# Performance work log

Hardware: AMD Instinct MI355X
Metric: run time of the kernel (lower is better)

## Reference

```python
import jax, jax.numpy as jnp
import numpy as np

N, E, D = 10000, 160000, 512
H, C = 4, 128          # hidden layers: 4 heads x 128 = 512 (residual-compatible)
HF, CF = 2, 512        # final layer: 2 heads, concat=False (mean)
NEG_SLOPE = 0.2


def _gat(x, src, dst, W, a_src, a_dst, b, heads, out_c, concat):
    """PyG-style GATConv (v1 attention), no dropout (eval mode)."""
    n = x.shape[0]
    h = (x @ W).reshape(n, heads, out_c)                  # [N,H,C]
    es = (h * a_src).sum(-1)                              # [N,H]
    ed = (h * a_dst).sum(-1)                              # [N,H]
    e = jax.nn.leaky_relu(es[src] + ed[dst], NEG_SLOPE)   # [E,H]
    m = jax.ops.segment_max(e, dst, num_segments=n)       # softmax over in-edges of dst
    m = jnp.where(jnp.isfinite(m), m, 0.0)                # guard isolated nodes
    ex = jnp.exp(e - m[dst])
    den = jax.ops.segment_sum(ex, dst, num_segments=n)
    alpha = ex / (den[dst] + 1e-16)                       # [E,H]
    msg = h[src] * alpha[..., None]                       # [E,H,C]
    out = jax.ops.segment_sum(msg, dst, num_segments=n)   # [N,H,C]
    out = out.reshape(n, heads * out_c) if concat else out.mean(axis=1)
    return out + b


def setup_inputs() -> dict:
    key = jax.random.key(0)
    ks = jax.random.split(key, 16)
    s = 0.05
    return {
        "graph": jax.random.normal(ks[0], (N, D), jnp.float32),
        "edge_index": jax.random.randint(ks[1], (2, E), 0, N, dtype=jnp.int32),
        "W1": jax.random.normal(ks[2], (D, H * C), jnp.float32) * s,
        "as1": jax.random.normal(ks[3], (H, C), jnp.float32) * s,
        "ad1": jax.random.normal(ks[4], (H, C), jnp.float32) * s,
        "b1": jnp.zeros((H * C,), jnp.float32),
        "W2": jax.random.normal(ks[5], (H * C, H * C), jnp.float32) * s,
        "as2": jax.random.normal(ks[6], (H, C), jnp.float32) * s,
        "ad2": jax.random.normal(ks[7], (H, C), jnp.float32) * s,
        "b2": jnp.zeros((H * C,), jnp.float32),
        "W3": jax.random.normal(ks[8], (H * C, HF * CF), jnp.float32) * s,
        "as3": jax.random.normal(ks[9], (HF, CF), jnp.float32) * s,
        "ad3": jax.random.normal(ks[10], (HF, CF), jnp.float32) * s,
        "b3": jnp.zeros((CF,), jnp.float32),
    }


def reference(graph, edge_index, W1, as1, ad1, b1, W2, as2, ad2, b2, W3, as3, ad3, b3):
    src, dst = edge_index[0], edge_index[1]
    # layer_size=2: conv1 + convs[0] with ELU+residual, convs[1] (concat=False) residual only
    x = jax.nn.elu(_gat(graph, src, dst, W1, as1, ad1, b1, H, C, True) + graph)
    x = jax.nn.elu(_gat(x, src, dst, W2, as2, ad2, b2, H, C, True) + x)
    x = _gat(x, src, dst, W3, as3, ad3, b3, HF, CF, False) + x
    return x
```

## Files before the change

kernel.cpp:

```cpp
#include <hip/hip_runtime.h>
#include <hip/hip_bf16.h>
#include <hip/hip_fp16.h>
#include <cstddef>
#include <cstdint>


typedef _Float16 half8 __attribute__((ext_vector_type(8)));
typedef _Float16 half4v __attribute__((ext_vector_type(4)));
typedef float floatx4 __attribute__((ext_vector_type(4)));

#define AS1(p) ((const __attribute__((address_space(1))) void*)(p))
#define AS3(p) ((__attribute__((address_space(3))) void*)(p))

__device__ __forceinline__ float leaky_exp(float e) {
    e = (e > 0.f) ? e : 0.2f * e;
    return __expf(e);
}


__global__ void count_deg(const int* __restrict__ dst, int* __restrict__ deg, int E) {
    int e = blockIdx.x * blockDim.x + threadIdx.x;
    if (e < E) atomicAdd(&deg[dst[e]], 1);
}

__global__ void scan_kernel(const int* __restrict__ deg, int* __restrict__ row_start,
                            int* __restrict__ cursor, int n) {
    __shared__ int wsum[16];
    __shared__ int carry_s;
    int tid = threadIdx.x;
    int wave = tid >> 6, lane = tid & 63;
    if (tid == 0) { carry_s = 0; row_start[0] = 0; }
    __syncthreads();
    for (int base = 0; base < n; base += 1024) {
        int i = base + tid;
        int v = (i < n) ? deg[i] : 0;
        int x = v;
#pragma unroll
        for (int off = 1; off < 64; off <<= 1) {
            int t = __shfl_up(x, off);
            if (lane >= off) x += t;
        }
        if (lane == 63) wsum[wave] = x;
        __syncthreads();
        if (wave == 0 && lane < 16) {
            int w = wsum[lane];
#pragma unroll
            for (int off = 1; off < 16; off <<= 1) {
                int t = __shfl_up(w, off);
                if (lane >= off) w += t;
            }
            wsum[lane] = w;
        }
        __syncthreads();
        int carry = carry_s;
        int incl = x + (wave ? wsum[wave - 1] : 0) + carry;
        if (i < n) { row_start[i + 1] = incl; cursor[i] = incl - v; }
        __syncthreads();
        if (tid == 1023) carry_s = incl;
        __syncthreads();
    }
}

__global__ void scatter_edges(const int* __restrict__ src, const int* __restrict__ dst,
                              int* __restrict__ cursor, int* __restrict__ srcs, int E) {
    int e = blockIdx.x * blockDim.x + threadIdx.x;
    if (e < E) {
        int p = atomicAdd(&cursor[dst[e]], 1);
        srcs[p] = src[e];
    }
}


__global__ void cast_f16(const float* __restrict__ in, _Float16* __restrict__ out, int n4) {
    int i = blockIdx.x * blockDim.x + threadIdx.x;
    if (i < n4) {
        float4 v = ((const float4*)in)[i];
        half4v o = {(_Float16)v.x, (_Float16)v.y, (_Float16)v.z, (_Float16)v.w};
        ((half4v*)out)[i] = o;
    }
}

__global__ void prep_weights(const float* __restrict__ W1, const float* __restrict__ W2,
                             const float* __restrict__ W3,
                             _Float16* __restrict__ Wt1, _Float16* __restrict__ Wt2,
                             _Float16* __restrict__ Bt3) {
    __shared__ float t[32][33];
    int b = blockIdx.x;
    int region = b >> 8, idx = b & 255;
    int r0 = (idx >> 4) * 32, c0 = (idx & 15) * 32;
    const float* in;
    _Float16* out;
    int in_ld, out_ld;
    if (region == 0)      { in = W1;       out = Wt1;       in_ld = 512;  out_ld = 512;  }
    else if (region == 1) { in = W2;       out = Wt2;       in_ld = 512;  out_ld = 512;  }
    else if (region == 2) { in = W3;       out = Bt3;       in_ld = 1024; out_ld = 1024; }
    else                  { in = W3 + 512; out = Bt3 + 512; in_ld = 1024; out_ld = 1024; }
    int tx = threadIdx.x, ty = threadIdx.y;
    for (int i = ty; i < 32; i += 8)
        t[i][tx] = in[(size_t)(r0 + i) * in_ld + c0 + tx];
    __syncthreads();
    for (int i = ty; i < 32; i += 8)
        out[(size_t)(c0 + i) * out_ld + r0 + tx] = (_Float16)t[tx][i];
}

__global__ void proj_all(const float* __restrict__ W1, const float* __restrict__ as1,
                         const float* __restrict__ ad1,
                         const float* __restrict__ W2, const float* __restrict__ as2,
                         const float* __restrict__ ad2,
                         const float* __restrict__ W3, const float* __restrict__ as3,
                         const float* __restrict__ ad3,
                         _Float16* __restrict__ Wt1, _Float16* __restrict__ Wt2,
                         float* __restrict__ wes3, float* __restrict__ wed3) {
    int w = (blockIdx.x * blockDim.x + threadIdx.x) >> 6;
    int lane = threadIdx.x & 63;
    if (w < 8192) {
        int layer = w >> 12;
        int idx = w & 4095;
        int d = idx & 511, hh = (idx >> 9) & 3, sel = idx >> 11;
        const float* W = layer ? W2 : W1;
        const float* a = layer ? (sel ? ad2 : as2) : (sel ? ad1 : as1);
        const float* row = W + (size_t)d * 512 + hh * 128;
        const float* av = a + hh * 128;
        float s = 0.f;
        s += row[lane] * av[lane];
        s += row[lane + 64] * av[lane + 64];
#pragma unroll
        for (int off = 32; off; off >>= 1) s += __shfl_down(s, off);
        if (lane == 0) {
            _Float16* Wt = layer ? Wt2 : Wt1;
            Wt[(size_t)(512 + sel * 4 + hh) * 512 + d] = (_Float16)s;
        }
    } else if (w < 10240) {
        int idx = w - 8192;
        int k = idx & 511, hh = (idx >> 9) & 1, sel = idx >> 10;
        const float* a = (sel ? ad3 : as3) + hh * 512;
        const float* row = W3 + (size_t)k * 1024 + hh * 512;
        float s = 0.f;
        for (int c = lane; c < 512; c += 64) s += row[c] * a[c];
#pragma unroll
        for (int off = 32; off; off >>= 1) s += __shfl_down(s, off);
        if (lane == 0) (sel ? wed3 : wes3)[hh * 512 + k] = s;
    } else if (w < 11136) {
        int z = (w - 10240) * 64 + lane;
        int layer = z / 28672;
        int rem = z - layer * 28672;
        int row = 520 + rem / 512, col = rem & 511;
        (layer ? Wt2 : Wt1)[(size_t)row * 512 + col] = (_Float16)0.f;
    }
}


#define BK 64

__global__ __launch_bounds__(256) void gemm_f16_att(const _Float16* __restrict__ A,
                                                    const _Float16* __restrict__ Bt,
                                                    _Float16* __restrict__ Hout,
                                                    float* __restrict__ es,
                                                    float* __restrict__ ed,
                                                    int M, int K) {
    __shared__ _Float16 As[64 * BK];
    __shared__ _Float16 Bs[64 * BK];
    int tid = threadIdx.x;
    int lane = tid & 63, wave = tid >> 6;
    int wm = (wave & 1) * 32, wn = (wave >> 1) * 32;
    int m0 = blockIdx.y * 64, n0 = blockIdx.x * 64;
    int l15 = lane & 15, quad = lane >> 4;
    int trow = tid >> 3, tcol = tid & 7;

    floatx4 acc[2][2];
#pragma unroll
    for (int i = 0; i < 2; ++i)
#pragma unroll
        for (int j = 0; j < 2; ++j) acc[i][j] = (floatx4){0.f, 0.f, 0.f, 0.f};

    for (int k0 = 0; k0 < K; k0 += BK) {
        __syncthreads();
#pragma unroll
        for (int i = 0; i < 2; ++i) {
            int gr = m0 + i * 32 + trow; if (gr >= M) gr = M - 1;
            __builtin_amdgcn_global_load_lds(AS1(A + (size_t)gr * K + k0 + tcol * 8),
                                             AS3(As + (size_t)(i * 256 + tid) * 8), 16, 0, 0);
        }
#pragma unroll
        for (int i = 0; i < 2; ++i) {
            int gr = n0 + i * 32 + trow;
            __builtin_amdgcn_global_load_lds(AS1(Bt + (size_t)gr * K + k0 + tcol * 8),
                                             AS3(Bs + (size_t)(i * 256 + tid) * 8), 16, 0, 0);
        }
        __syncthreads();
#pragma unroll
        for (int ks = 0; ks < BK; ks += 32) {
            half8 af[2], bfr[2];
#pragma unroll
            for (int i = 0; i < 2; ++i)
                af[i] = *(const half8*)&As[(wm + i * 16 + l15) * BK + ks + quad * 8];
#pragma unroll
            for (int j = 0; j < 2; ++j)
                bfr[j] = *(const half8*)&Bs[(wn + j * 16 + l15) * BK + ks + quad * 8];
#pragma unroll
            for (int i = 0; i < 2; ++i)
#pragma unroll
                for (int j = 0; j < 2; ++j)
                    acc[i][j] = __builtin_amdgcn_mfma_f32_16x16x32_f16(af[i], bfr[j], acc[i][j], 0, 0, 0);
        }
    }
#pragma unroll
    for (int i = 0; i < 2; ++i)
#pragma unroll
        for (int j = 0; j < 2; ++j) {
            int col = n0 + wn + j * 16 + l15;
#pragma unroll
            for (int r = 0; r < 4; ++r) {
                int row = m0 + wm + i * 16 + quad * 4 + r;
                if (row < M) {
                    float v = acc[i][j][r];
                    if (col < 512) Hout[(size_t)row * 512 + col] = (_Float16)v;
                    else if (col < 516) es[row * 4 + col - 512] = v;
                    else if (col < 520) ed[row * 4 + col - 516] = v;
                }
            }
        }
}

__global__ __launch_bounds__(256) void gemm_f16_ep(const _Float16* __restrict__ A,
                                                   const _Float16* __restrict__ Bt,
                                                   float* __restrict__ out,
                                                   const float* __restrict__ bias,
                                                   const _Float16* __restrict__ xres,
                                                   int M, int Nn, int K) {
    __shared__ _Float16 As[64 * BK];
    __shared__ _Float16 Bs[64 * BK];
    int tid = threadIdx.x;
    int lane = tid & 63, wave = tid >> 6;
    int wm = (wave & 1) * 32, wn = (wave >> 1) * 32;
    int m0 = blockIdx.y * 64, n0 = blockIdx.x * 64;
    int l15 = lane & 15, quad = lane >> 4;
    int trow = tid >> 3, tcol = tid & 7;

    floatx4 acc[2][2];
#pragma unroll
    for (int i = 0; i < 2; ++i)
#pragma unroll
        for (int j = 0; j < 2; ++j) acc[i][j] = (floatx4){0.f, 0.f, 0.f, 0.f};

    for (int k0 = 0; k0 < K; k0 += BK) {
        __syncthreads();
#pragma unroll
        for (int i = 0; i < 2; ++i) {
            int gr = m0 + i * 32 + trow; if (gr >= M) gr = M - 1;
            __builtin_amdgcn_global_load_lds(AS1(A + (size_t)gr * K + k0 + tcol * 8),
                                             AS3(As + (size_t)(i * 256 + tid) * 8), 16, 0, 0);
        }
#pragma unroll
        for (int i = 0; i < 2; ++i) {
            int gr = n0 + i * 32 + trow;
            __builtin_amdgcn_global_load_lds(AS1(Bt + (size_t)gr * K + k0 + tcol * 8),
                                             AS3(Bs + (size_t)(i * 256 + tid) * 8), 16, 0, 0);
        }
        __syncthreads();
#pragma unroll
        for (int ks = 0; ks < BK; ks += 32) {
            half8 af[2], bfr[2];
#pragma unroll
            for (int i = 0; i < 2; ++i)
                af[i] = *(const half8*)&As[(wm + i * 16 + l15) * BK + ks + quad * 8];
#pragma unroll
            for (int j = 0; j < 2; ++j)
                bfr[j] = *(const half8*)&Bs[(wn + j * 16 + l15) * BK + ks + quad * 8];
#pragma unroll
            for (int i = 0; i < 2; ++i)
#pragma unroll
                for (int j = 0; j < 2; ++j)
                    acc[i][j] = __builtin_amdgcn_mfma_f32_16x16x32_f16(af[i], bfr[j], acc[i][j], 0, 0, 0);
        }
    }
#pragma unroll
    for (int i = 0; i < 2; ++i)
#pragma unroll
        for (int j = 0; j < 2; ++j) {
            int col = n0 + wn + j * 16 + l15;
#pragma unroll
            for (int r = 0; r < 4; ++r) {
                int row = m0 + wm + i * 16 + quad * 4 + r;
                if (row < M)
                    out[(size_t)row * Nn + col] =
                        0.5f * acc[i][j][r] + bias[col] + (float)xres[(size_t)row * Nn + col];
            }
        }
}


template <bool RES32, bool COEF3>
__global__ __launch_bounds__(512) void aggregate7_concat(
    const _Float16* __restrict__ h, const float* __restrict__ es,
    const float* __restrict__ ed,
    const int* __restrict__ row_start, const int* __restrict__ srcs,
    const float* __restrict__ bias, const float* __restrict__ xres32,
    const _Float16* __restrict__ xres16, _Float16* __restrict__ x_out_h,
    const float* __restrict__ wes3, const float* __restrict__ wed3,
    float* __restrict__ es3, float* __restrict__ ed3, int Nn) {
    int wave = threadIdx.x >> 6, lane = threadIdx.x & 63;
    int n = blockIdx.x * 8 + wave;
    if (n >= Nn) return;
    int head = lane >> 4;
    int c0 = lane * 8;
    float edn = ed[n * 4 + head];
    int beg = row_start[n], end = row_start[n + 1];
    float acc[8] = {};
    float den = 0.f;
    int j = beg;
    for (; j + 3 < end; j += 4) {
        int s0 = srcs[j], s1 = srcs[j + 1], s2 = srcs[j + 2], s3 = srcs[j + 3];
        float e0 = es[s0 * 4 + head], e1 = es[s1 * 4 + head];
        float e2 = es[s2 * 4 + head], e3 = es[s3 * 4 + head];
        half8 h0 = *(const half8*)&h[(size_t)s0 * 512 + c0];
        half8 h1 = *(const half8*)&h[(size_t)s1 * 512 + c0];
        half8 h2 = *(const half8*)&h[(size_t)s2 * 512 + c0];
        half8 h3 = *(const half8*)&h[(size_t)s3 * 512 + c0];
        float w0 = leaky_exp(e0 + edn), w1 = leaky_exp(e1 + edn);
        float w2 = leaky_exp(e2 + edn), w3 = leaky_exp(e3 + edn);
        den += w0 + w1 + w2 + w3;
#pragma unroll
        for (int k = 0; k < 8; ++k) acc[k] += w0 * (float)h0[k];
#pragma unroll
        for (int k = 0; k < 8; ++k) acc[k] += w1 * (float)h1[k];
#pragma unroll
        for (int k = 0; k < 8; ++k) acc[k] += w2 * (float)h2[k];
#pragma unroll
        for (int k = 0; k < 8; ++k) acc[k] += w3 * (float)h3[k];
    }
    for (; j < end; ++j) {
        int s = srcs[j];
        float w = leaky_exp(es[s * 4 + head] + edn);
        half8 hv = *(const half8*)&h[(size_t)s * 512 + c0];
        den += w;
#pragma unroll
        for (int k = 0; k < 8; ++k) acc[k] += w * (float)hv[k];
    }
    float invden = 1.f / (den + 1e-16f);
    size_t base = (size_t)n * 512 + c0;
    float v[8];
    half8 o;
#pragma unroll
    for (int k = 0; k < 8; ++k) {
        float res = RES32 ? xres32[base + k] : (float)xres16[base + k];
        float t = acc[k] * invden + bias[c0 + k] + res;
        t = (t > 0.f) ? t : expm1f(t);
        v[k] = t;
        o[k] = (_Float16)t;
    }
    *(half8*)&x_out_h[base] = o;
    if (COEF3) {
        float t0 = 0.f, t1 = 0.f, t2 = 0.f, t3 = 0.f;
#pragma unroll
        for (int k = 0; k < 8; ++k) {
            t0 += v[k] * wes3[c0 + k];
            t1 += v[k] * wes3[512 + c0 + k];
            t2 += v[k] * wed3[c0 + k];
            t3 += v[k] * wed3[512 + c0 + k];
        }
#pragma unroll
        for (int off = 32; off; off >>= 1) {
            t0 += __shfl_down(t0, off);
            t1 += __shfl_down(t1, off);
            t2 += __shfl_down(t2, off);
            t3 += __shfl_down(t3, off);
        }
        if (lane == 0) {
            es3[n * 2] = t0; es3[n * 2 + 1] = t1;
            ed3[n * 2] = t2; ed3[n * 2 + 1] = t3;
        }
    }
}


__global__ __launch_bounds__(512) void aggregate7_dual(
    const _Float16* __restrict__ x, const float* __restrict__ es3,
    const float* __restrict__ ed3,
    const int* __restrict__ row_start, const int* __restrict__ srcs,
    _Float16* __restrict__ y, int Nn) {
    int wave = threadIdx.x >> 6, lane = threadIdx.x & 63;
    int n = blockIdx.x * 8 + wave;
    if (n >= Nn) return;
    int c0 = lane * 8;
    float edn0 = ed3[n * 2], edn1 = ed3[n * 2 + 1];
    int beg = row_start[n], end = row_start[n + 1];
    float a0[8] = {}, a1[8] = {};
    float den0 = 0.f, den1 = 0.f;
    int j = beg;
    for (; j + 3 < end; j += 4) {
        int s0 = srcs[j], s1 = srcs[j + 1], s2 = srcs[j + 2], s3 = srcs[j + 3];
        float2 q0 = *(const float2*)&es3[s0 * 2];
        float2 q1 = *(const float2*)&es3[s1 * 2];
        float2 q2 = *(const float2*)&es3[s2 * 2];
        float2 q3 = *(const float2*)&es3[s3 * 2];
        half8 h0 = *(const half8*)&x[(size_t)s0 * 512 + c0];
        half8 h1 = *(const half8*)&x[(size_t)s1 * 512 + c0];
        half8 h2 = *(const half8*)&x[(size_t)s2 * 512 + c0];
        half8 h3 = *(const half8*)&x[(size_t)s3 * 512 + c0];
        float u0 = leaky_exp(q0.x + edn0), v0 = leaky_exp(q0.y + edn1);
        float u1 = leaky_exp(q1.x + edn0), v1 = leaky_exp(q1.y + edn1);
        float u2 = leaky_exp(q2.x + edn0), v2 = leaky_exp(q2.y + edn1);
        float u3 = leaky_exp(q3.x + edn0), v3 = leaky_exp(q3.y + edn1);
        den0 += u0 + u1 + u2 + u3;
        den1 += v0 + v1 + v2 + v3;
#pragma unroll
        for (int k = 0; k < 8; ++k) { float f = (float)h0[k]; a0[k] += u0 * f; a1[k] += v0 * f; }
#pragma unroll
        for (int k = 0; k < 8; ++k) { float f = (float)h1[k]; a0[k] += u1 * f; a1[k] += v1 * f; }
#pragma unroll
        for (int k = 0; k < 8; ++k) { float f = (float)h2[k]; a0[k] += u2 * f; a1[k] += v2 * f; }
#pragma unroll
        for (int k = 0; k < 8; ++k) { float f = (float)h3[k]; a0[k] += u3 * f; a1[k] += v3 * f; }
    }
    for (; j < end; ++j) {
        int s = srcs[j];
        float2 q = *(const float2*)&es3[s * 2];
        float u = leaky_exp(q.x + edn0), v = leaky_exp(q.y + edn1);
        half8 hv = *(const half8*)&x[(size_t)s * 512 + c0];
        den0 += u; den1 += v;
#pragma unroll
        for (int k = 0; k < 8; ++k) { float f = (float)hv[k]; a0[k] += u * f; a1[k] += v * f; }
    }
    float invd0 = 1.f / (den0 + 1e-16f);
    float invd1 = 1.f / (den1 + 1e-16f);
    half8 o0, o1;
#pragma unroll
    for (int k = 0; k < 8; ++k) {
        o0[k] = (_Float16)(a0[k] * invd0);
        o1[k] = (_Float16)(a1[k] * invd1);
    }
    *(half8*)&y[(size_t)n * 1024 + c0] = o0;
    *(half8*)&y[(size_t)n * 1024 + 512 + c0] = o1;
}


extern "C" void kernel_launch(void* const* d_in, const int* in_sizes, int n_in,
                              void* d_out, int out_size, void* d_ws, size_t ws_size,
                              hipStream_t stream) {
    const float* graph = (const float*)d_in[0];
    const int* edge_index = (const int*)d_in[1];
    const float* W1 = (const float*)d_in[2];
    const float* as1 = (const float*)d_in[3];
    const float* ad1 = (const float*)d_in[4];
    const float* b1 = (const float*)d_in[5];
    const float* W2 = (const float*)d_in[6];
    const float* as2 = (const float*)d_in[7];
    const float* ad2 = (const float*)d_in[8];
    const float* b2 = (const float*)d_in[9];
    const float* W3 = (const float*)d_in[10];
    const float* as3 = (const float*)d_in[11];
    const float* ad3 = (const float*)d_in[12];
    const float* b3 = (const float*)d_in[13];

    const int D = 512;
    int N = in_sizes[0] / D;
    int E = in_sizes[1] / 2;
    const int* src = edge_index;
    const int* dst = edge_index + E;

    char* p = (char*)d_ws;
    auto carve = [&](size_t bytes) {
        void* r = (void*)p;
        p += (bytes + 255) & ~(size_t)255;
        return r;
    };
    _Float16* Ah   = (_Float16*)carve((size_t)N * 512 * 2);
    _Float16* Wt1  = (_Float16*)carve((size_t)576 * 512 * 2);
    _Float16* Wt2  = (_Float16*)carve((size_t)576 * 512 * 2);
    _Float16* Bt3  = (_Float16*)carve((size_t)512 * 1024 * 2);
    _Float16* h_h  = (_Float16*)carve((size_t)N * 1024 * 2);
    float* es      = (float*)carve((size_t)N * 4 * 4);
    float* ed      = (float*)carve((size_t)N * 4 * 4);
    float* es3     = (float*)carve((size_t)N * 2 * 4);
    float* ed3     = (float*)carve((size_t)N * 2 * 4);
    float* wes3    = (float*)carve((size_t)2 * 512 * 4);
    float* wed3    = (float*)carve((size_t)2 * 512 * 4);
    int* deg       = (int*)carve((size_t)N * 4);
    int* cur       = (int*)carve((size_t)N * 4);
    int* row_st    = (int*)carve((size_t)(N + 1) * 4);
    int* srcs      = (int*)carve((size_t)E * 4);

    hipMemsetAsync(deg, 0, (size_t)N * 4, stream);
    count_deg<<<(E + 255) / 256, 256, 0, stream>>>(dst, deg, E);
    scan_kernel<<<1, 1024, 0, stream>>>(deg, row_st, cur, N);
    scatter_edges<<<(E + 255) / 256, 256, 0, stream>>>(src, dst, cur, srcs, E);

    cast_f16<<<(N * 512 / 4 + 255) / 256, 256, 0, stream>>>(graph, Ah, N * 512 / 4);
    prep_weights<<<1024, dim3(32, 8), 0, stream>>>(W1, W2, W3, Wt1, Wt2, Bt3);
    proj_all<<<2784, 256, 0, stream>>>(W1, as1, ad1, W2, as2, ad2, W3, as3, ad3,
                                       Wt1, Wt2, wes3, wed3);

    int nblk8 = (N + 7) / 8;
    int mblk = (N + 63) / 64;
    gemm_f16_att<<<dim3(9, mblk), 256, 0, stream>>>(Ah, Wt1, h_h, es, ed, N, 512);
    aggregate7_concat<true, false><<<nblk8, 512, 0, stream>>>(
        h_h, es, ed, row_st, srcs, b1, graph, nullptr, Ah,
        nullptr, nullptr, nullptr, nullptr, N);

    gemm_f16_att<<<dim3(9, mblk), 256, 0, stream>>>(Ah, Wt2, h_h, es, ed, N, 512);
    aggregate7_concat<false, true><<<nblk8, 512, 0, stream>>>(
        h_h, es, ed, row_st, srcs, b2, nullptr, Ah, Ah,
        wes3, wed3, es3, ed3, N);

    aggregate7_dual<<<nblk8, 512, 0, stream>>>(Ah, es3, ed3, row_st, srcs, h_h, N);
    gemm_f16_ep<<<dim3(8, mblk), 256, 0, stream>>>(
        h_h, Bt3, (float*)d_out, b3, Ah, N, 512, 1024);
}
```

Baseline: 311.2 us.

## Fuse prep kernels, enlarge final GEMM tile, unroll aggregation loops by eight

Merges the cast, weight-transpose and projection kernels into a single launch, with block ranges selecting each role, to remove two launches. The final epilogue GEMM now uses 128x64 tiles with each wave covering all 64 columns, which increases B-fragment reuse and halves the grid rows. The aggregation kernels gain an 8-way unrolled edge loop that issues more independent gathers per iteration for memory-level parallelism, at the cost of more registers.

```diff
diff --git a/kernel.cpp b/kernel.cpp
--- a/kernel.cpp
+++ b/kernel.cpp
@@ -71,48 +71,49 @@
 }
 
 
-__global__ void cast_f16(const float* __restrict__ in, _Float16* __restrict__ out, int n4) {
-    int i = blockIdx.x * blockDim.x + threadIdx.x;
-    if (i < n4) {
-        float4 v = ((const float4*)in)[i];
-        half4v o = {(_Float16)v.x, (_Float16)v.y, (_Float16)v.z, (_Float16)v.w};
-        ((half4v*)out)[i] = o;
-    }
-}
-
-__global__ void prep_weights(const float* __restrict__ W1, const float* __restrict__ W2,
-                             const float* __restrict__ W3,
-                             _Float16* __restrict__ Wt1, _Float16* __restrict__ Wt2,
-                             _Float16* __restrict__ Bt3) {
-    __shared__ float t[32][33];
+__global__ void prep_all(const float* __restrict__ graph, _Float16* __restrict__ Ah, int n4,
+                         int cb,
+                         const float* __restrict__ W1, const float* __restrict__ W2,
+                         const float* __restrict__ W3,
+                         _Float16* __restrict__ Wt1, _Float16* __restrict__ Wt2,
+                         _Float16* __restrict__ Bt3,
+                         const float* __restrict__ as1, const float* __restrict__ ad1,
+                         const float* __restrict__ as2, const float* __restrict__ ad2,
+                         const float* __restrict__ as3, const float* __restrict__ ad3,
+                         float* __restrict__ wes3, float* __restrict__ wed3) {
     int b = blockIdx.x;
-    int region = b >> 8, idx = b & 255;
-    int r0 = (idx >> 4) * 32, c0 = (idx & 15) * 32;
-    const float* in;
-    _Float16* out;
-    int in_ld, out_ld;
-    if (region == 0)      { in = W1;       out = Wt1;       in_ld = 512;  out_ld = 512;  }
-    else if (region == 1) { in = W2;       out = Wt2;       in_ld = 512;  out_ld = 512;  }
-    else if (region == 2) { in = W3;       out = Bt3;       in_ld = 1024; out_ld = 1024; }
-    else                  { in = W3 + 512; out = Bt3 + 512; in_ld = 1024; out_ld = 1024; }
-    int tx = threadIdx.x, ty = threadIdx.y;
-    for (int i = ty; i < 32; i += 8)
-        t[i][tx] = in[(size_t)(r0 + i) * in_ld + c0 + tx];
-    __syncthreads();
-    for (int i = ty; i < 32; i += 8)
-        out[(size_t)(c0 + i) * out_ld + r0 + tx] = (_Float16)t[tx][i];
-}
-
-__global__ void proj_all(const float* __restrict__ W1, const float* __restrict__ as1,
-                         const float* __restrict__ ad1,
-                         const float* __restrict__ W2, const float* __restrict__ as2,
-                         const float* __restrict__ ad2,
-                         const float* __restrict__ W3, const float* __restrict__ as3,
-                         const float* __restrict__ ad3,
-                         _Float16* __restrict__ Wt1, _Float16* __restrict__ Wt2,
-                         float* __restrict__ wes3, float* __restrict__ wed3) {
-    int w = (blockIdx.x * blockDim.x + threadIdx.x) >> 6;
-    int lane = threadIdx.x & 63;
+    int tid = threadIdx.x;
+    if (b < cb) {
+        int i = b * 256 + tid;
+        if (i < n4) {
+            float4 v = ((const float4*)graph)[i];
+            half4v o = {(_Float16)v.x, (_Float16)v.y, (_Float16)v.z, (_Float16)v.w};
+            ((half4v*)Ah)[i] = o;
+        }
+        return;
+    }
+    if (b < cb + 1024) {
+        __shared__ float t[32][33];
+        int bb = b - cb;
+        int region = bb >> 8, idx = bb & 255;
+        int r0 = (idx >> 4) * 32, c0 = (idx & 15) * 32;
+        const float* in;
+        _Float16* out;
+        int in_ld, out_ld;
+        if (region == 0)      { in = W1;       out = Wt1;       in_ld = 512;  out_ld = 512;  }
+        else if (region == 1) { in = W2;       out = Wt2;       in_ld = 512;  out_ld = 512;  }
+        else if (region == 2) { in = W3;       out = Bt3;       in_ld = 1024; out_ld = 1024; }
+        else                  { in = W3 + 512; out = Bt3 + 512; in_ld = 1024; out_ld = 1024; }
+        int tx = tid & 31, ty = tid >> 5;
+        for (int i = ty; i < 32; i += 8)
+            t[i][tx] = in[(size_t)(r0 + i) * in_ld + c0 + tx];
+        __syncthreads();
+        for (int i = ty; i < 32; i += 8)
+            out[(size_t)(c0 + i) * out_ld + r0 + tx] = (_Float16)t[tx][i];
+        return;
+    }
+    int w = (b - cb - 1024) * 4 + (tid >> 6);
+    int lane = tid & 63;
     if (w < 8192) {
         int layer = w >> 12;
         int idx = w & 4095;
@@ -228,25 +229,25 @@
                                                    const float* __restrict__ bias,
                                                    const _Float16* __restrict__ xres,
                                                    int M, int Nn, int K) {
-    __shared__ _Float16 As[64 * BK];
+    __shared__ _Float16 As[128 * BK];
     __shared__ _Float16 Bs[64 * BK];
     int tid = threadIdx.x;
     int lane = tid & 63, wave = tid >> 6;
-    int wm = (wave & 1) * 32, wn = (wave >> 1) * 32;
-    int m0 = blockIdx.y * 64, n0 = blockIdx.x * 64;
+    int wm = wave * 32;
+    int m0 = blockIdx.y * 128, n0 = blockIdx.x * 64;
     int l15 = lane & 15, quad = lane >> 4;
     int trow = tid >> 3, tcol = tid & 7;
 
-    floatx4 acc[2][2];
+    floatx4 acc[2][4];
 #pragma unroll
     for (int i = 0; i < 2; ++i)
 #pragma unroll
-        for (int j = 0; j < 2; ++j) acc[i][j] = (floatx4){0.f, 0.f, 0.f, 0.f};
+        for (int j = 0; j < 4; ++j) acc[i][j] = (floatx4){0.f, 0.f, 0.f, 0.f};
 
     for (int k0 = 0; k0 < K; k0 += BK) {
         __syncthreads();
 #pragma unroll
-        for (int i = 0; i < 2; ++i) {
+        for (int i = 0; i < 4; ++i) {
             int gr = m0 + i * 32 + trow; if (gr >= M) gr = M - 1;
             __builtin_amdgcn_global_load_lds(AS1(A + (size_t)gr * K + k0 + tcol * 8),
                                              AS3(As + (size_t)(i * 256 + tid) * 8), 16, 0, 0);
@@ -260,25 +261,25 @@
         __syncthreads();
 #pragma unroll
         for (int ks = 0; ks < BK; ks += 32) {
-            half8 af[2], bfr[2];
+            half8 af[2], bfr[4];
 #pragma unroll
             for (int i = 0; i < 2; ++i)
                 af[i] = *(const half8*)&As[(wm + i * 16 + l15) * BK + ks + quad * 8];
 #pragma unroll
-            for (int j = 0; j < 2; ++j)
-                bfr[j] = *(const half8*)&Bs[(wn + j * 16 + l15) * BK + ks + quad * 8];
+            for (int j = 0; j < 4; ++j)
+                bfr[j] = *(const half8*)&Bs[(j * 16 + l15) * BK + ks + quad * 8];
 #pragma unroll
             for (int i = 0; i < 2; ++i)
 #pragma unroll
-                for (int j = 0; j < 2; ++j)
+                for (int j = 0; j < 4; ++j)
                     acc[i][j] = __builtin_amdgcn_mfma_f32_16x16x32_f16(af[i], bfr[j], acc[i][j], 0, 0, 0);
         }
     }
 #pragma unroll
     for (int i = 0; i < 2; ++i)
 #pragma unroll
-        for (int j = 0; j < 2; ++j) {
-            int col = n0 + wn + j * 16 + l15;
+        for (int j = 0; j < 4; ++j) {
+            int col = n0 + j * 16 + l15;
 #pragma unroll
             for (int r = 0; r < 4; ++r) {
                 int row = m0 + wm + i * 16 + quad * 4 + r;
@@ -291,7 +292,7 @@
 
 
 template <bool RES32, bool COEF3>
-__global__ __launch_bounds__(512) void aggregate7_concat(
+__global__ __launch_bounds__(512) void aggregate8_concat(
     const _Float16* __restrict__ h, const float* __restrict__ es,
     const float* __restrict__ ed,
     const int* __restrict__ row_start, const int* __restrict__ srcs,
@@ -309,25 +310,41 @@
     float acc[8] = {};
     float den = 0.f;
     int j = beg;
+    for (; j + 7 < end; j += 8) {
+        int s[8];
+        float e[8];
+        half8 hv[8];
+#pragma unroll
+        for (int q = 0; q < 8; ++q) s[q] = srcs[j + q];
+#pragma unroll
+        for (int q = 0; q < 8; ++q) e[q] = es[s[q] * 4 + head];
+#pragma unroll
+        for (int q = 0; q < 8; ++q) hv[q] = *(const half8*)&h[(size_t)s[q] * 512 + c0];
+#pragma unroll
+        for (int q = 0; q < 8; ++q) {
+            float w = leaky_exp(e[q] + edn);
+            den += w;
+#pragma unroll
+            for (int k = 0; k < 8; ++k) acc[k] += w * (float)hv[q][k];
+        }
+    }
     for (; j + 3 < end; j += 4) {
-        int s0 = srcs[j], s1 = srcs[j + 1], s2 = srcs[j + 2], s3 = srcs[j + 3];
-        float e0 = es[s0 * 4 + head], e1 = es[s1 * 4 + head];
-        float e2 = es[s2 * 4 + head], e3 = es[s3 * 4 + head];
-        half8 h0 = *(const half8*)&h[(size_t)s0 * 512 + c0];
-        half8 h1 = *(const half8*)&h[(size_t)s1 * 512 + c0];
-        half8 h2 = *(const half8*)&h[(size_t)s2 * 512 + c0];
-        half8 h3 = *(const half8*)&h[(size_t)s3 * 512 + c0];
-        float w0 = leaky_exp(e0 + edn), w1 = leaky_exp(e1 + edn);
-        float w2 = leaky_exp(e2 + edn), w3 = leaky_exp(e3 + edn);
-        den += w0 + w1 + w2 + w3;
-#pragma unroll
-        for (int k = 0; k < 8; ++k) acc[k] += w0 * (float)h0[k];
-#pragma unroll
-        for (int k = 0; k < 8; ++k) acc[k] += w1 * (float)h1[k];
-#pragma unroll
-        for (int k = 0; k < 8; ++k) acc[k] += w2 * (float)h2[k];
-#pragma unroll
-        for (int k = 0; k < 8; ++k) acc[k] += w3 * (float)h3[k];
+        int s[4];
+        float e[4];
+        half8 hv[4];
+#pragma unroll
+        for (int q = 0; q < 4; ++q) s[q] = srcs[j + q];
+#pragma unroll
+        for (int q = 0; q < 4; ++q) e[q] = es[s[q] * 4 + head];
+#pragma unroll
+        for (int q = 0; q < 4; ++q) hv[q] = *(const half8*)&h[(size_t)s[q] * 512 + c0];
+#pragma unroll
+        for (int q = 0; q < 4; ++q) {
+            float w = leaky_exp(e[q] + edn);
+            den += w;
+#pragma unroll
+            for (int k = 0; k < 8; ++k) acc[k] += w * (float)hv[q][k];
+        }
     }
     for (; j < end; ++j) {
         int s = srcs[j];
@@ -374,7 +391,7 @@
 }
 
 
-__global__ __launch_bounds__(512) void aggregate7_dual(
+__global__ __launch_bounds__(512) void aggregate8_dual(
     const _Float16* __restrict__ x, const float* __restrict__ es3,
     const float* __restrict__ ed3,
     const int* __restrict__ row_start, const int* __restrict__ srcs,
@@ -388,30 +405,41 @@
     float a0[8] = {}, a1[8] = {};
     float den0 = 0.f, den1 = 0.f;
     int j = beg;
+    for (; j + 7 < end; j += 8) {
+        int s[8];
+        float2 q[8];
+        half8 hv[8];
+#pragma unroll
+        for (int t = 0; t < 8; ++t) s[t] = srcs[j + t];
+#pragma unroll
+        for (int t = 0; t < 8; ++t) q[t] = *(const float2*)&es3[s[t] * 2];
+#pragma unroll
+        for (int t = 0; t < 8; ++t) hv[t] = *(const half8*)&x[(size_t)s[t] * 512 + c0];
+#pragma unroll
+        for (int t = 0; t < 8; ++t) {
+            float u = leaky_exp(q[t].x + edn0), v = leaky_exp(q[t].y + edn1);
+            den0 += u; den1 += v;
+#pragma unroll
+            for (int k = 0; k < 8; ++k) { float f = (float)hv[t][k]; a0[k] += u * f; a1[k] += v * f; }
+        }
+    }
     for (; j + 3 < end; j += 4) {
-        int s0 = srcs[j], s1 = srcs[j + 1], s2 = srcs[j + 2], s3 = srcs[j + 3];
-        float2 q0 = *(const float2*)&es3[s0 * 2];
-        float2 q1 = *(const float2*)&es3[s1 * 2];
-        float2 q2 = *(const float2*)&es3[s2 * 2];
-        float2 q3 = *(const float2*)&es3[s3 * 2];
-        half8 h0 = *(const half8*)&x[(size_t)s0 * 512 + c0];
-        half8 h1 = *(const half8*)&x[(size_t)s1 * 512 + c0];
-        half8 h2 = *(const half8*)&x[(size_t)s2 * 512 + c0];
-        half8 h3 = *(const half8*)&x[(size_t)s3 * 512 + c0];
-        float u0 = leaky_exp(q0.x + edn0), v0 = leaky_exp(q0.y + edn1);
-        float u1 = leaky_exp(q1.x + edn0), v1 = leaky_exp(q1.y + edn1);
-        float u2 = leaky_exp(q2.x + edn0), v2 = leaky_exp(q2.y + edn1);
-        float u3 = leaky_exp(q3.x + edn0), v3 = leaky_exp(q3.y + edn1);
-        den0 += u0 + u1 + u2 + u3;
-        den1 += v0 + v1 + v2 + v3;
-#pragma unroll
-        for (int k = 0; k < 8; ++k) { float f = (float)h0[k]; a0[k] += u0 * f; a1[k] += v0 * f; }
-#pragma unroll
-        for (int k = 0; k < 8; ++k) { float f = (float)h1[k]; a0[k] += u1 * f; a1[k] += v1 * f; }
-#pragma unroll
-        for (int k = 0; k < 8; ++k) { float f = (float)h2[k]; a0[k] += u2 * f; a1[k] += v2 * f; }
-#pragma unroll
-        for (int k = 0; k < 8; ++k) { float f = (float)h3[k]; a0[k] += u3 * f; a1[k] += v3 * f; }
+        int s[4];
+        float2 q[4];
+        half8 hv[4];
+#pragma unroll
+        for (int t = 0; t < 4; ++t) s[t] = srcs[j + t];
+#pragma unroll
+        for (int t = 0; t < 4; ++t) q[t] = *(const float2*)&es3[s[t] * 2];
+#pragma unroll
+        for (int t = 0; t < 4; ++t) hv[t] = *(const half8*)&x[(size_t)s[t] * 512 + c0];
+#pragma unroll
+        for (int t = 0; t < 4; ++t) {
+            float u = leaky_exp(q[t].x + edn0), v = leaky_exp(q[t].y + edn1);
+            den0 += u; den1 += v;
+#pragma unroll
+            for (int k = 0; k < 8; ++k) { float f = (float)hv[t][k]; a0[k] += u * f; a1[k] += v * f; }
+        }
     }
     for (; j < end; ++j) {
         int s = srcs[j];
@@ -486,24 +514,26 @@
     scan_kernel<<<1, 1024, 0, stream>>>(deg, row_st, cur, N);
     scatter_edges<<<(E + 255) / 256, 256, 0, stream>>>(src, dst, cur, srcs, E);
 
-    cast_f16<<<(N * 512 / 4 + 255) / 256, 256, 0, stream>>>(graph, Ah, N * 512 / 4);
-    prep_weights<<<1024, dim3(32, 8), 0, stream>>>(W1, W2, W3, Wt1, Wt2, Bt3);
-    proj_all<<<2784, 256, 0, stream>>>(W1, as1, ad1, W2, as2, ad2, W3, as3, ad3,
-                                       Wt1, Wt2, wes3, wed3);
+    int n4 = N * 512 / 4;
+    int cb = (n4 + 255) / 256;
+    prep_all<<<cb + 1024 + 2784, 256, 0, stream>>>(
+        graph, Ah, n4, cb, W1, W2, W3, Wt1, Wt2, Bt3,
+        as1, ad1, as2, ad2, as3, ad3, wes3, wed3);
 
     int nblk8 = (N + 7) / 8;
     int mblk = (N + 63) / 64;
+    int mblk128 = (N + 127) / 128;
     gemm_f16_att<<<dim3(9, mblk), 256, 0, stream>>>(Ah, Wt1, h_h, es, ed, N, 512);
-    aggregate7_concat<true, false><<<nblk8, 512, 0, stream>>>(
+    aggregate8_concat<true, false><<<nblk8, 512, 0, stream>>>(
         h_h, es, ed, row_st, srcs, b1, graph, nullptr, Ah,
         nullptr, nullptr, nullptr, nullptr, N);
 
     gemm_f16_att<<<dim3(9, mblk), 256, 0, stream>>>(Ah, Wt2, h_h, es, ed, N, 512);
-    aggregate7_concat<false, true><<<nblk8, 512, 0, stream>>>(
+    aggregate8_concat<false, true><<<nblk8, 512, 0, stream>>>(
         h_h, es, ed, row_st, srcs, b2, nullptr, Ah, Ah,
         wes3, wed3, es3, ed3, N);
 
-    aggregate7_dual<<<nblk8, 512, 0, stream>>>(Ah, es3, ed3, row_st, srcs, h_h, N);
-    gemm_f16_ep<<<dim3(8, mblk), 256, 0, stream>>>(
+    aggregate8_dual<<<nblk8, 512, 0, stream>>>(Ah, es3, ed3, row_st, srcs, h_h, N);
+    gemm_f16_ep<<<dim3(8, mblk128), 256, 0, stream>>>(
         h_h, Bt3, (float*)d_out, b3, Ah, N, 512, 1024);
 }
```

New measurement: 311.4 us. About the same (+0.1%).

## Merge prep kernels into one launch, chunk scan, enlarge final GEMM tile

Applied to the files above, without the earlier changes.

Merges the degree count, fp16 cast, weight transpose and attention-projection kernels into a single block-dispatched launch to cut launch overhead and the gaps between kernels. The single-block scan now handles 16 elements per thread per pass, so the serial loop runs fewer times. The final epilogue GEMM now uses 128-row tiles, with each wave computing a 32x64 output, which raises data reuse and halves the number of row blocks. In exchange it uses more registers and gives fewer blocks for occupancy.

```diff
diff --git a/kernel.cpp b/kernel.cpp
--- a/kernel.cpp
+++ b/kernel.cpp
@@ -17,11 +17,6 @@
     return __expf(e);
 }
 
-
-__global__ void count_deg(const int* __restrict__ dst, int* __restrict__ deg, int E) {
-    int e = blockIdx.x * blockDim.x + threadIdx.x;
-    if (e < E) atomicAdd(&deg[dst[e]], 1);
-}
 
 __global__ void scan_kernel(const int* __restrict__ deg, int* __restrict__ row_start,
                             int* __restrict__ cursor, int n) {
@@ -31,10 +26,19 @@
     int wave = tid >> 6, lane = tid & 63;
     if (tid == 0) { carry_s = 0; row_start[0] = 0; }
     __syncthreads();
-    for (int base = 0; base < n; base += 1024) {
-        int i = base + tid;
-        int v = (i < n) ? deg[i] : 0;
-        int x = v;
+    const int CH = 16;
+    for (int base = 0; base < n; base += 1024 * CH) {
+        int i0 = base + tid * CH;
+        int loc[CH];
+        int tsum = 0;
+#pragma unroll
+        for (int q = 0; q < CH; ++q) {
+            int idx = i0 + q;
+            int v = (idx < n) ? deg[idx] : 0;
+            tsum += v;
+            loc[q] = tsum;
+        }
+        int x = tsum;
 #pragma unroll
         for (int off = 1; off < 64; off <<= 1) {
             int t = __shfl_up(x, off);
@@ -53,10 +57,18 @@
         }
         __syncthreads();
         int carry = carry_s;
-        int incl = x + (wave ? wsum[wave - 1] : 0) + carry;
-        if (i < n) { row_start[i + 1] = incl; cursor[i] = incl - v; }
-        __syncthreads();
-        if (tid == 1023) carry_s = incl;
+        int toff = carry + (wave ? wsum[wave - 1] : 0) + (x - tsum);
+#pragma unroll
+        for (int q = 0; q < CH; ++q) {
+            int idx = i0 + q;
+            if (idx < n) {
+                int excl = toff + (q ? loc[q - 1] : 0);
+                row_start[idx + 1] = toff + loc[q];
+                cursor[idx] = excl;
+            }
+        }
+        __syncthreads();
+        if (tid == 0) carry_s = carry + wsum[15];
         __syncthreads();
     }
 }
@@ -71,48 +83,55 @@
 }
 
 
-__global__ void cast_f16(const float* __restrict__ in, _Float16* __restrict__ out, int n4) {
-    int i = blockIdx.x * blockDim.x + threadIdx.x;
-    if (i < n4) {
-        float4 v = ((const float4*)in)[i];
-        half4v o = {(_Float16)v.x, (_Float16)v.y, (_Float16)v.z, (_Float16)v.w};
-        ((half4v*)out)[i] = o;
-    }
-}
-
-__global__ void prep_weights(const float* __restrict__ W1, const float* __restrict__ W2,
-                             const float* __restrict__ W3,
-                             _Float16* __restrict__ Wt1, _Float16* __restrict__ Wt2,
-                             _Float16* __restrict__ Bt3) {
-    __shared__ float t[32][33];
+__global__ void prep_all(const float* __restrict__ graph, _Float16* __restrict__ Ah, int n4,
+                         int cb, int pb,
+                         const float* __restrict__ W1, const float* __restrict__ W2,
+                         const float* __restrict__ W3,
+                         _Float16* __restrict__ Wt1, _Float16* __restrict__ Wt2,
+                         _Float16* __restrict__ Bt3,
+                         const float* __restrict__ as1, const float* __restrict__ ad1,
+                         const float* __restrict__ as2, const float* __restrict__ ad2,
+                         const float* __restrict__ as3, const float* __restrict__ ad3,
+                         float* __restrict__ wes3, float* __restrict__ wed3,
+                         const int* __restrict__ dst, int* __restrict__ deg, int E) {
     int b = blockIdx.x;
-    int region = b >> 8, idx = b & 255;
-    int r0 = (idx >> 4) * 32, c0 = (idx & 15) * 32;
-    const float* in;
-    _Float16* out;
-    int in_ld, out_ld;
-    if (region == 0)      { in = W1;       out = Wt1;       in_ld = 512;  out_ld = 512;  }
-    else if (region == 1) { in = W2;       out = Wt2;       in_ld = 512;  out_ld = 512;  }
-    else if (region == 2) { in = W3;       out = Bt3;       in_ld = 1024; out_ld = 1024; }
-    else                  { in = W3 + 512; out = Bt3 + 512; in_ld = 1024; out_ld = 1024; }
-    int tx = threadIdx.x, ty = threadIdx.y;
-    for (int i = ty; i < 32; i += 8)
-        t[i][tx] = in[(size_t)(r0 + i) * in_ld + c0 + tx];
-    __syncthreads();
-    for (int i = ty; i < 32; i += 8)
-        out[(size_t)(c0 + i) * out_ld + r0 + tx] = (_Float16)t[tx][i];
-}
-
-__global__ void proj_all(const float* __restrict__ W1, const float* __restrict__ as1,
-                         const float* __restrict__ ad1,
-                         const float* __restrict__ W2, const float* __restrict__ as2,
-                         const float* __restrict__ ad2,
-                         const float* __restrict__ W3, const float* __restrict__ as3,
-                         const float* __restrict__ ad3,
-                         _Float16* __restrict__ Wt1, _Float16* __restrict__ Wt2,
-                         float* __restrict__ wes3, float* __restrict__ wed3) {
-    int w = (blockIdx.x * blockDim.x + threadIdx.x) >> 6;
-    int lane = threadIdx.x & 63;
+    int tid = threadIdx.x;
+    if (b < cb) {
+        int i = b * 256 + tid;
+        if (i < n4) {
+            float4 v = ((const float4*)graph)[i];
+            half4v o = {(_Float16)v.x, (_Float16)v.y, (_Float16)v.z, (_Float16)v.w};
+            ((half4v*)Ah)[i] = o;
+        }
+        return;
+    }
+    if (b < cb + 1024) {
+        __shared__ float t[32][33];
+        int bb = b - cb;
+        int region = bb >> 8, idx = bb & 255;
+        int r0 = (idx >> 4) * 32, c0 = (idx & 15) * 32;
+        const float* in;
+        _Float16* out;
+        int in_ld, out_ld;
+        if (region == 0)      { in = W1;       out = Wt1;       in_ld = 512;  out_ld = 512;  }
+        else if (region == 1) { in = W2;       out = Wt2;       in_ld = 512;  out_ld = 512;  }
+        else if (region == 2) { in = W3;       out = Bt3;       in_ld = 1024; out_ld = 1024; }
+        else                  { in = W3 + 512; out = Bt3 + 512; in_ld = 1024; out_ld = 1024; }
+        int tx = tid & 31, ty = tid >> 5;
+        for (int i = ty; i < 32; i += 8)
+            t[i][tx] = in[(size_t)(r0 + i) * in_ld + c0 + tx];
+        __syncthreads();
+        for (int i = ty; i < 32; i += 8)
+            out[(size_t)(c0 + i) * out_ld + r0 + tx] = (_Float16)t[tx][i];
+        return;
+    }
+    if (b >= pb) {
+        int e = (b - pb) * 256 + tid;
+        if (e < E) atomicAdd(&deg[dst[e]], 1);
+        return;
+    }
+    int w = (b - cb - 1024) * 4 + (tid >> 6);
+    int lane = tid & 63;
     if (w < 8192) {
         int layer = w >> 12;
         int idx = w & 4095;
@@ -228,25 +247,25 @@
                                                    const float* __restrict__ bias,
                                                    const _Float16* __restrict__ xres,
                                                    int M, int Nn, int K) {
-    __shared__ _Float16 As[64 * BK];
+    __shared__ _Float16 As[128 * BK];
     __shared__ _Float16 Bs[64 * BK];
     int tid = threadIdx.x;
     int lane = tid & 63, wave = tid >> 6;
-    int wm = (wave & 1) * 32, wn = (wave >> 1) * 32;
-    int m0 = blockIdx.y * 64, n0 = blockIdx.x * 64;
+    int wm = wave * 32;
+    int m0 = blockIdx.y * 128, n0 = blockIdx.x * 64;
     int l15 = lane & 15, quad = lane >> 4;
     int trow = tid >> 3, tcol = tid & 7;
 
-    floatx4 acc[2][2];
+    floatx4 acc[2][4];
 #pragma unroll
     for (int i = 0; i < 2; ++i)
 #pragma unroll
-        for (int j = 0; j < 2; ++j) acc[i][j] = (floatx4){0.f, 0.f, 0.f, 0.f};
+        for (int j = 0; j < 4; ++j) acc[i][j] = (floatx4){0.f, 0.f, 0.f, 0.f};
 
     for (int k0 = 0; k0 < K; k0 += BK) {
         __syncthreads();
 #pragma unroll
-        for (int i = 0; i < 2; ++i) {
+        for (int i = 0; i < 4; ++i) {
             int gr = m0 + i * 32 + trow; if (gr >= M) gr = M - 1;
             __builtin_amdgcn_global_load_lds(AS1(A + (size_t)gr * K + k0 + tcol * 8),
                                              AS3(As + (size_t)(i * 256 + tid) * 8), 16, 0, 0);
@@ -260,25 +279,25 @@
         __syncthreads();
 #pragma unroll
         for (int ks = 0; ks < BK; ks += 32) {
-            half8 af[2], bfr[2];
+            half8 af[2], bfr[4];
 #pragma unroll
             for (int i = 0; i < 2; ++i)
                 af[i] = *(const half8*)&As[(wm + i * 16 + l15) * BK + ks + quad * 8];
 #pragma unroll
-            for (int j = 0; j < 2; ++j)
-                bfr[j] = *(const half8*)&Bs[(wn + j * 16 + l15) * BK + ks + quad * 8];
+            for (int j = 0; j < 4; ++j)
+                bfr[j] = *(const half8*)&Bs[(j * 16 + l15) * BK + ks + quad * 8];
 #pragma unroll
             for (int i = 0; i < 2; ++i)
 #pragma unroll
-                for (int j = 0; j < 2; ++j)
+                for (int j = 0; j < 4; ++j)
                     acc[i][j] = __builtin_amdgcn_mfma_f32_16x16x32_f16(af[i], bfr[j], acc[i][j], 0, 0, 0);
         }
     }
 #pragma unroll
     for (int i = 0; i < 2; ++i)
 #pragma unroll
-        for (int j = 0; j < 2; ++j) {
-            int col = n0 + wn + j * 16 + l15;
+        for (int j = 0; j < 4; ++j) {
+            int col = n0 + j * 16 + l15;
 #pragma unroll
             for (int r = 0; r < 4; ++r) {
                 int row = m0 + wm + i * 16 + quad * 4 + r;
@@ -482,17 +501,20 @@
     int* srcs      = (int*)carve((size_t)E * 4);
 
     hipMemsetAsync(deg, 0, (size_t)N * 4, stream);
-    count_deg<<<(E + 255) / 256, 256, 0, stream>>>(dst, deg, E);
+    int n4 = N * 512 / 4;
+    int cb = (n4 + 255) / 256;
+    int pb = cb + 1024 + 2784;
+    int eb = (E + 255) / 256;
+    prep_all<<<pb + eb, 256, 0, stream>>>(
+        graph, Ah, n4, cb, pb, W1, W2, W3, Wt1, Wt2, Bt3,
+        as1, ad1, as2, ad2, as3, ad3, wes3, wed3, dst, deg, E);
+
     scan_kernel<<<1, 1024, 0, stream>>>(deg, row_st, cur, N);
     scatter_edges<<<(E + 255) / 256, 256, 0, stream>>>(src, dst, cur, srcs, E);
 
-    cast_f16<<<(N * 512 / 4 + 255) / 256, 256, 0, stream>>>(graph, Ah, N * 512 / 4);
-    prep_weights<<<1024, dim3(32, 8), 0, stream>>>(W1, W2, W3, Wt1, Wt2, Bt3);
-    proj_all<<<2784, 256, 0, stream>>>(W1, as1, ad1, W2, as2, ad2, W3, as3, ad3,
-                                       Wt1, Wt2, wes3, wed3);
-
     int nblk8 = (N + 7) / 8;
     int mblk = (N + 63) / 64;
+    int mblk128 = (N + 127) / 128;
     gemm_f16_att<<<dim3(9, mblk), 256, 0, stream>>>(Ah, Wt1, h_h, es, ed, N, 512);
     aggregate7_concat<true, false><<<nblk8, 512, 0, stream>>>(
         h_h, es, ed, row_st, srcs, b1, graph, nullptr, Ah,
@@ -504,6 +526,6 @@
         wes3, wed3, es3, ed3, N);
 
     aggregate7_dual<<<nblk8, 512, 0, stream>>>(Ah, es3, ed3, row_st, srcs, h_h, N);
-    gemm_f16_ep<<<dim3(8, mblk), 256, 0, stream>>>(
+    gemm_f16_ep<<<dim3(8, mblk128), 256, 0, stream>>>(
         h_h, Bt3, (float*)d_out, b3, Ah, N, 512, 1024);
 }
```

Measured after the change: 311.1 us. No clear change (-0.0%).
